# Kernel optimization log

Hardware: AMD Instinct MI355X
Metric: run time of the kernel (lower is better)

Reference implementation:

```python
import jax, jax.numpy as jnp
import numpy as np

B = 1024      # batch of seed nodes
S = 16        # sample_size
H = 256       # hidden
IN = 150      # in_dim + NUM_CLASS (128 + 22)
OUT = 22
HEADS = 8
NN = 100000   # number of graph nodes
LN_EPS = 1e-5


def setup_inputs() -> dict:
    key = jax.random.key(0)
    ks = jax.random.split(key, 16)
    sc = 0.05
    return {
        "node_feats": jax.random.normal(ks[0], (NN, IN), jnp.float32),
        "batch": jax.random.randint(ks[1], (B,), 0, NN),
        "nbr2": jax.random.randint(ks[2], (B, S), 0, NN),
        "nbr1": jax.random.randint(ks[3], (B * (S + 1), S), 0, NN),
        "W_in": jax.random.normal(ks[4], (IN, H), jnp.float32) * sc,
        "b_in": jnp.zeros((H,), jnp.float32),
        "Wqkv": jax.random.normal(ks[5], (2, 3, H, H), jnp.float32) * sc,
        "bqkv": jnp.zeros((2, 3, H), jnp.float32),
        "Wo": jax.random.normal(ks[6], (2, H, H), jnp.float32) * sc,
        "bo": jnp.zeros((2, H), jnp.float32),
        "Wf": jax.random.normal(ks[7], (2, H, H), jnp.float32) * sc,
        "bf": jnp.zeros((2, H), jnp.float32),
        "ln_g": jnp.ones((4, H), jnp.float32),
        "ln_b": jnp.zeros((4, H), jnp.float32),
        "W_out": jax.random.normal(ks[8], (H, OUT), jnp.float32) * sc,
        "b_out": jnp.zeros((OUT,), jnp.float32),
    }


def _layer_norm(x, g, b):
    m = jnp.mean(x, axis=-1, keepdims=True)
    v = jnp.mean((x - m) ** 2, axis=-1, keepdims=True)
    return (x - m) * jax.lax.rsqrt(v + LN_EPS) * g + b


def _mha(q, kv, Wq, Wk, Wv, bq, bk, bv, Wout, bout):
    # q: [N, 1, H], kv: [N, S, H]; single-query multi-head attention
    N, Sk, _ = kv.shape
    dh = H // HEADS
    qp = (q @ Wq + bq).reshape(N, 1, HEADS, dh)
    kp = (kv @ Wk + bk).reshape(N, Sk, HEADS, dh)
    vp = (kv @ Wv + bv).reshape(N, Sk, HEADS, dh)
    att = jax.nn.softmax(
        jnp.einsum("nqhd,nkhd->nhqk", qp, kp) / np.float32(np.sqrt(dh)), axis=-1
    )
    o = jnp.einsum("nhqk,nkhd->nqhd", att, vp).reshape(N, 1, H)
    return o @ Wout + bout


def _attn_block(x, l, Wqkv, bqkv, Wo, bo, Wf, bf, ln_g, ln_b):
    # x: [N, S+1, H]; slot 0 is the query (self), rest are sampled neighbors
    q, kv = x[:, 0:1, :], x[:, 1:, :]
    h = _mha(q, kv, Wqkv[l, 0], Wqkv[l, 1], Wqkv[l, 2],
             bqkv[l, 0], bqkv[l, 1], bqkv[l, 2], Wo[l], bo[l])
    h = h[:, 0, :] + q[:, 0, :]                       # residual
    h = _layer_norm(h, ln_g[2 * l], ln_b[2 * l])
    h = h + (h @ Wf[l] + bf[l])                       # FFN (single Linear) + residual
    return _layer_norm(h, ln_g[2 * l + 1], ln_b[2 * l + 1])


def reference(node_feats, batch, nbr2, nbr1, W_in, b_in, Wqkv, bqkv, Wo, bo,
              Wf, bf, ln_g, ln_b, W_out, b_out):
    # Recursive neighbor expansion (unrolled for layers=2)
    ids1 = jnp.concatenate([batch[:, None], nbr2], axis=1).reshape(-1)   # [B*(S+1)]
    ids0 = jnp.concatenate([ids1[:, None], nbr1], axis=1).reshape(-1)    # [B*(S+1)^2]
    # layer 0: proj_in(features) = ReLU(Linear) (Dropout identity in eval)
    h0 = jax.nn.relu(node_feats[ids0] @ W_in + b_in)                     # [M0, H]
    # layer 1
    h1 = _attn_block(h0.reshape(B * (S + 1), S + 1, H), 0,
                     Wqkv, bqkv, Wo, bo, Wf, bf, ln_g, ln_b)
    # layer 2
    h2 = _attn_block(h1.reshape(B, S + 1, H), 1,
                     Wqkv, bqkv, Wo, bo, Wf, bf, ln_g, ln_b)
    # proj_out: Linear -> Softmax
    return jax.nn.softmax(h2 @ W_out + b_out, axis=-1)
```

## Files before the change

### kernel.cpp

```cpp
#include <hip/hip_runtime.h>
#include <hip/hip_bf16.h>
#include <math.h>

typedef unsigned short ushort_t;
typedef __bf16 bf16x8 __attribute__((ext_vector_type(8)));
typedef float  f32x4  __attribute__((ext_vector_type(4)));

#define B_SZ   1024
#define SEQ    17
#define KVN    16
#define HDIM   256
#define NHEAD  8
#define DH     32
#define INF    150
#define OUTD   22
#define LN_EPS 1e-5f
#define N1     (B_SZ * SEQ)
#define NN_    100000
#define NKVBLK 1563
#define NHQBLK 272

constexpr size_t SZ_H0    = (size_t)NN_ * 256 * 2;
constexpr size_t SZ_KV0   = (size_t)NN_ * 512 * 2;
constexpr size_t SZ_ROW   = (size_t)N1 * 256 * 2;
constexpr size_t OFF_HQ   = 0;
constexpr size_t OFF_KV0  = OFF_HQ + SZ_H0;
constexpr size_t OFF_QKV1 = OFF_KV0;
constexpr size_t OFF_O1   = OFF_QKV1 + (size_t)N1 * 768 * 2;
constexpr size_t OFF_HA2  = OFF_O1 + (size_t)B_SZ * 256 * 2;
constexpr size_t OFF_H2   = OFF_HA2 + (size_t)B_SZ * 256 * 2;
constexpr size_t OFF_Q0   = OFF_KV0 + SZ_KV0;
constexpr size_t OFF_O0   = OFF_Q0 + SZ_ROW;
constexpr size_t OFF_H1   = OFF_O0;
constexpr size_t OFF_HA   = OFF_O0 + SZ_ROW;
constexpr size_t OFF_IDS  = OFF_HA + SZ_ROW;
constexpr size_t OFF_WTIN = OFF_IDS + (size_t)N1 * 4;
constexpr size_t OFF_WKV0 = OFF_WTIN + 256 * 160 * 2;
constexpr size_t OFF_WQ0  = OFF_WKV0 + 512 * 256 * 2;
constexpr size_t OFF_WKVQ1= OFF_WQ0 + 256 * 256 * 2;
constexpr size_t OFF_WO0  = OFF_WKVQ1 + 768 * 256 * 2;
constexpr size_t OFF_WF0  = OFF_WO0 + 256 * 256 * 2;
constexpr size_t OFF_WO1  = OFF_WF0 + 256 * 256 * 2;
constexpr size_t OFF_WF1  = OFF_WO1 + 256 * 256 * 2;
constexpr size_t OFF_B1   = OFF_WF1 + 256 * 256 * 2;

__device__ __forceinline__ ushort_t f2bfu(float x) {
    __hip_bfloat16 h = __float2bfloat16(x);
    return *reinterpret_cast<ushort_t*>(&h);
}
__device__ __forceinline__ float bfu2f(ushort_t u) {
    __hip_bfloat16 h;
    *reinterpret_cast<ushort_t*>(&h) = u;
    return __bfloat162float(h);
}
__device__ __forceinline__ f32x4 mfma16(bf16x8 a, bf16x8 b, f32x4 c) {
    return __builtin_amdgcn_mfma_f32_16x16x32_bf16(a, b, c, 0, 0, 0);
}

__global__ __launch_bounds__(256) void k_prep(
    const float* __restrict__ W_in, const float* __restrict__ Wqkv,
    const float* __restrict__ Wo, const float* __restrict__ Wf,
    const float* __restrict__ bqkv,
    const int* __restrict__ batch, const int* __restrict__ nbr2,
    char* __restrict__ ws) {
    const int job = blockIdx.y;
    const int idx = blockIdx.x * 256 + threadIdx.x;
    if (job == 11) {
        if (idx < N1) {
            int b = idx / SEQ, s = idx % SEQ;
            ((int*)(ws + OFF_IDS))[idx] = (s == 0) ? batch[b] : nbr2[b * KVN + s - 1];
        }
        return;
    }
    if (job == 12) {
        if (idx < 768) ((float*)(ws + OFF_B1))[idx] = bqkv[768 + ((idx + 256) % 768)];
        return;
    }
    const float* src = nullptr; ushort_t* dst = nullptr;
    int Kpad = 256, Kvalid = 256;
    switch (job) {
        case 0:  src = W_in;           dst = (ushort_t*)(ws + OFF_WTIN); Kpad = 160; Kvalid = 150; break;
        case 1:  src = Wqkv + 65536;   dst = (ushort_t*)(ws + OFF_WKV0); break;
        case 2:  src = Wqkv + 131072;  dst = (ushort_t*)(ws + OFF_WKV0) + 65536; break;
        case 3:  src = Wqkv;           dst = (ushort_t*)(ws + OFF_WQ0); break;
        case 4:  src = Wqkv + 262144;  dst = (ushort_t*)(ws + OFF_WKVQ1); break;
        case 5:  src = Wqkv + 327680;  dst = (ushort_t*)(ws + OFF_WKVQ1) + 65536; break;
        case 6:  src = Wqkv + 196608;  dst = (ushort_t*)(ws + OFF_WKVQ1) + 131072; break;
        case 7:  src = Wo;             dst = (ushort_t*)(ws + OFF_WO0); break;
        case 8:  src = Wo + 65536;     dst = (ushort_t*)(ws + OFF_WO1); break;
        case 9:  src = Wf;             dst = (ushort_t*)(ws + OFF_WF0); break;
        case 10: src = Wf + 65536;     dst = (ushort_t*)(ws + OFF_WF1); break;
    }
    const int total = 256 * Kpad;
    if (idx >= total) return;
    int n = idx / Kpad, k = idx % Kpad;
    dst[idx] = (k < Kvalid) ? f2bfu(src[(size_t)k * 256 + n]) : (ushort_t)0;
}

__global__ __launch_bounds__(256) void k_fused(
    const float* __restrict__ nf,
    const ushort_t* __restrict__ Wt_in, const float* __restrict__ b_in,
    const ushort_t* __restrict__ Wkv, const ushort_t* __restrict__ Wq,
    const float* __restrict__ bqkv, const int* __restrict__ ids1,
    ushort_t* __restrict__ kv0, ushort_t* __restrict__ hq,
    ushort_t* __restrict__ q0) {
    __shared__ ushort_t Ah[64 * 256];
    __shared__ ushort_t Sh[4][32][72];
    const int tid = threadIdx.x;
    const bool iskv = blockIdx.x < NKVBLK;
    const int m0 = (iskv ? blockIdx.x : blockIdx.x - NKVBLK) * 64;
    const int lane = tid & 63, w = tid >> 6;
    const int lr = lane & 15, q4 = lane >> 4, lk = q4 * 8;

    {
        ushort_t (*Astage)[168] = reinterpret_cast<ushort_t (*)[168]>(Ah);
        #pragma unroll
        for (int i = 0; i < 5; ++i) {
            int flat = tid + i * 256;
            int row = flat / 20, ch = flat % 20;
            int gm; bool valid;
            if (iskv) { gm = m0 + row; valid = gm < NN_; if (!valid) gm = 0; }
            else      { gm = ids1[m0 + row]; valid = true; }
            const float* ap = nf + (size_t)gm * INF + ch * 8;
            ushort_t tmp[8];
            if (valid && ch < 18) {
                #pragma unroll
                for (int j = 0; j < 4; ++j) {
                    float2 f = *reinterpret_cast<const float2*>(ap + j * 2);
                    tmp[j * 2] = f2bfu(f.x); tmp[j * 2 + 1] = f2bfu(f.y);
                }
            } else {
                #pragma unroll
                for (int j = 0; j < 8; ++j) {
                    int k = ch * 8 + j;
                    tmp[j] = (valid && k < INF) ? f2bfu(ap[j]) : (ushort_t)0;
                }
            }
            *reinterpret_cast<int4*>(&Astage[row][ch * 8]) = *reinterpret_cast<int4*>(tmp);
        }
    }
    __syncthreads();

    f32x4 acc[4][4] = {};
    {
        ushort_t (*Astage)[168] = reinterpret_cast<ushort_t (*)[168]>(Ah);
        #pragma unroll 2
        for (int s = 0; s < 5; ++s) {
            bf16x8 a[4], b[4];
            #pragma unroll
            for (int mi = 0; mi < 4; ++mi)
                a[mi] = *reinterpret_cast<const bf16x8*>(&Astage[mi * 16 + lr][s * 32 + lk]);
            #pragma unroll
            for (int ni = 0; ni < 4; ++ni)
                b[ni] = *reinterpret_cast<const bf16x8*>(
                    Wt_in + (size_t)(w * 64 + ni * 16 + lr) * 160 + s * 32 + lk);
            #pragma unroll
            for (int mi = 0; mi < 4; ++mi)
                #pragma unroll
                for (int ni = 0; ni < 4; ++ni)
                    acc[mi][ni] = mfma16(a[mi], b[ni], acc[mi][ni]);
        }
    }
    __syncthreads();

    #pragma unroll
    for (int ni = 0; ni < 4; ++ni) {
        int col = w * 64 + ni * 16 + lr;
        float bb = b_in[col];
        #pragma unroll
        for (int mi = 0; mi < 4; ++mi)
            #pragma unroll
            for (int r = 0; r < 4; ++r) {
                int row = mi * 16 + q4 * 4 + r;
                Ah[row * 256 + (col ^ ((row & 7) << 3))] =
                    f2bfu(fmaxf(acc[mi][ni][r] + bb, 0.f));
            }
    }
    __syncthreads();

    if (!iskv) {
        #pragma unroll
        for (int i = 0; i < 8; ++i) {
            int flat = tid + i * 256;
            int row = flat >> 5, ch = flat & 31;
            *reinterpret_cast<int4*>(hq + (size_t)(m0 + row) * 256 + ch * 8) =
                *reinterpret_cast<const int4*>(&Ah[row * 256 + (ch ^ (row & 7)) * 8]);
        }
    }

    const int nh = iskv ? 2 : 1;
    for (int h = 0; h < nh; ++h) {
        const ushort_t* Bm = iskv ? (Wkv + (size_t)h * 256 * 256) : Wq;
        const float* bias = iskv ? (bqkv + 256 + h * 256) : bqkv;
        f32x4 acc2[4][4] = {};
        #pragma unroll 2
        for (int s = 0; s < 8; ++s) {
            bf16x8 a[4], b[4];
            #pragma unroll
            for (int mi = 0; mi < 4; ++mi) {
                int row = mi * 16 + lr;
                int chunk = (s * 4 + q4) ^ (row & 7);
                a[mi] = *reinterpret_cast<const bf16x8*>(&Ah[row * 256 + chunk * 8]);
            }
            #pragma unroll
            for (int ni = 0; ni < 4; ++ni)
                b[ni] = *reinterpret_cast<const bf16x8*>(
                    Bm + (size_t)(w * 64 + ni * 16 + lr) * 256 + s * 32 + lk);
            #pragma unroll
            for (int mi = 0; mi < 4; ++mi)
                #pragma unroll
                for (int ni = 0; ni < 4; ++ni)
                    acc2[mi][ni] = mfma16(a[mi], b[ni], acc2[mi][ni]);
        }
        float bl[4];
        #pragma unroll
        for (int ni = 0; ni < 4; ++ni) bl[ni] = bias[w * 64 + ni * 16 + lr];
        ushort_t* outp = iskv ? kv0 : q0;
        const int ldo = iskv ? 512 : 256;
        const int coff = (iskv ? h * 256 : 0) + w * 64;
        #pragma unroll
        for (int part = 0; part < 2; ++part) {
            #pragma unroll
            for (int mi2 = 0; mi2 < 2; ++mi2) {
                int mi = part * 2 + mi2;
                #pragma unroll
                for (int ni = 0; ni < 4; ++ni)
                    #pragma unroll
                    for (int r = 0; r < 4; ++r)
                        Sh[w][mi2 * 16 + q4 * 4 + r][ni * 16 + lr] =
                            f2bfu(acc2[mi][ni][r] + bl[ni]);
            }
            #pragma unroll
            for (int j = 0; j < 4; ++j) {
                int flat = lane + j * 64;
                int r32 = flat >> 3, ch = flat & 7;
                int grow = m0 + part * 32 + r32;
                if (!iskv || grow < NN_)
                    *reinterpret_cast<int4*>(outp + (size_t)grow * ldo + coff + ch * 8) =
                        *reinterpret_cast<const int4*>(&Sh[w][r32][ch * 8]);
            }
        }
    }
}

template<bool RELU>
__global__ __launch_bounds__(256) void gemm64(
    const ushort_t* __restrict__ Asrc, const ushort_t* __restrict__ Bt,
    const float* __restrict__ biasN, ushort_t* __restrict__ out,
    int M, int Ksteps, int lda, int ldb, int ldo,
    const int* __restrict__ arid) {
    __shared__ ushort_t Al[64][40];
    __shared__ ushort_t Bl[64][40];
    const int tid = threadIdx.x;
    const int m0 = blockIdx.x * 64, n0 = blockIdx.y * 64;
    const int lane = tid & 63, w = tid >> 6, wm = w >> 1, wn = w & 1;
    const int srow = tid >> 2, sch = tid & 3;
    const int gmi = m0 + srow;
    const bool valid = gmi < M;
    const int gr = valid ? (arid ? arid[gmi] : gmi) : 0;
    const ushort_t* arow = Asrc + (size_t)gr * lda + sch * 8;
    const ushort_t* brow = Bt + (size_t)(n0 + srow) * ldb + sch * 8;

    int4 aP = {0, 0, 0, 0};
    if (valid) aP = *reinterpret_cast<const int4*>(arow);
    int4 bP = *reinterpret_cast<const int4*>(brow);

    f32x4 acc[2][2] = {};
    for (int s = 0; s < Ksteps; ++s) {
        __syncthreads();
        *reinterpret_cast<int4*>(&Al[srow][sch * 8]) = aP;
        *reinterpret_cast<int4*>(&Bl[srow][sch * 8]) = bP;
        if (s + 1 < Ksteps) {
            if (valid) aP = *reinterpret_cast<const int4*>(arow + (s + 1) * 32);
            bP = *reinterpret_cast<const int4*>(brow + (s + 1) * 32);
        }
        __syncthreads();
        const int lr = lane & 15, lk = (lane >> 4) * 8;
        bf16x8 a0 = *reinterpret_cast<const bf16x8*>(&Al[wm * 32 + lr][lk]);
        bf16x8 a1 = *reinterpret_cast<const bf16x8*>(&Al[wm * 32 + 16 + lr][lk]);
        bf16x8 b0 = *reinterpret_cast<const bf16x8*>(&Bl[wn * 32 + lr][lk]);
        bf16x8 b1 = *reinterpret_cast<const bf16x8*>(&Bl[wn * 32 + 16 + lr][lk]);
        acc[0][0] = mfma16(a0, b0, acc[0][0]);
        acc[0][1] = mfma16(a0, b1, acc[0][1]);
        acc[1][0] = mfma16(a1, b0, acc[1][0]);
        acc[1][1] = mfma16(a1, b1, acc[1][1]);
    }
    #pragma unroll
    for (int mi = 0; mi < 2; ++mi)
        #pragma unroll
        for (int ni = 0; ni < 2; ++ni)
            #pragma unroll
            for (int r = 0; r < 4; ++r) {
                int m = m0 + wm * 32 + mi * 16 + ((lane >> 4) << 2) + r;
                int n = n0 + wn * 32 + ni * 16 + (lane & 15);
                if (m < M) {
                    float v = acc[mi][ni][r] + biasN[n];
                    if (RELU) v = fmaxf(v, 0.f);
                    out[(size_t)m * ldo + n] = f2bfu(v);
                }
            }
}

__global__ __launch_bounds__(256) void gemm_ln(
    const ushort_t* __restrict__ A, const ushort_t* __restrict__ Bt,
    const float* __restrict__ biasN,
    const ushort_t* __restrict__ resmat, const int* __restrict__ residx, int rstride,
    const float* __restrict__ lng, const float* __restrict__ lnb,
    ushort_t* __restrict__ out, int M) {
    __shared__ union {
        struct { ushort_t Al[32][264]; ushort_t Bl[256][40]; } s;
        struct { float xr[32][260]; float mrow[32]; float rrow[32]; int sidx[32]; } e;
    } sm;
    const int tid = threadIdx.x;
    const int m0 = blockIdx.x * 32;
    const int lane = tid & 63, w = tid >> 6;
    const int lr = lane & 15, lk = (lane >> 4) * 8;

    #pragma unroll
    for (int j = 0; j < 4; ++j) {
        int flat = tid + j * 256;
        int row = flat >> 5, ch = flat & 31;
        *reinterpret_cast<int4*>(&sm.s.Al[row][ch * 8]) =
            *reinterpret_cast<const int4*>(A + (size_t)(m0 + row) * 256 + ch * 8);
    }
    const ushort_t* brow = Bt + (size_t)tid * 256;
    int4 bP[4];
    #pragma unroll
    for (int j = 0; j < 4; ++j) bP[j] = *reinterpret_cast<const int4*>(brow + j * 8);

    f32x4 acc[2][4] = {};
    for (int s = 0; s < 8; ++s) {
        __syncthreads();
        #pragma unroll
        for (int j = 0; j < 4; ++j)
            *reinterpret_cast<int4*>(&sm.s.Bl[tid][j * 8]) = bP[j];
        if (s < 7) {
            #pragma unroll
            for (int j = 0; j < 4; ++j)
                bP[j] = *reinterpret_cast<const int4*>(brow + (s + 1) * 32 + j * 8);
        }
        __syncthreads();
        bf16x8 a0 = *reinterpret_cast<const bf16x8*>(&sm.s.Al[lr][s * 32 + lk]);
        bf16x8 a1 = *reinterpret_cast<const bf16x8*>(&sm.s.Al[16 + lr][s * 32 + lk]);
        #pragma unroll
        for (int ni = 0; ni < 4; ++ni) {
            bf16x8 b = *reinterpret_cast<const bf16x8*>(&sm.s.Bl[w * 64 + ni * 16 + lr][lk]);
            acc[0][ni] = mfma16(a0, b, acc[0][ni]);
            acc[1][ni] = mfma16(a1, b, acc[1][ni]);
        }
    }
    __syncthreads();
    if (tid < 32) sm.e.sidx[tid] = residx ? residx[m0 + tid] : (m0 + tid) * rstride;
    #pragma unroll
    for (int mi = 0; mi < 2; ++mi)
        #pragma unroll
        for (int ni = 0; ni < 4; ++ni)
            #pragma unroll
            for (int r = 0; r < 4; ++r) {
                int rl = mi * 16 + ((lane >> 4) << 2) + r;
                int cl = w * 64 + ni * 16 + (lane & 15);
                sm.e.xr[rl][cl] = acc[mi][ni][r];
            }
    __syncthreads();
    {
        float bn = biasN[tid];
        for (int r = 0; r < 32; ++r)
            sm.e.xr[r][tid] += bn + bfu2f(resmat[(size_t)sm.e.sidx[r] * 256 + tid]);
    }
    __syncthreads();
    {
        for (int rr = w * 8; rr < w * 8 + 8; ++rr) {
            float4 v = *reinterpret_cast<const float4*>(&sm.e.xr[rr][lane * 4]);
            float s1 = v.x + v.y + v.z + v.w;
            float s2 = v.x * v.x + v.y * v.y + v.z * v.z + v.w * v.w;
            #pragma unroll
            for (int off = 32; off > 0; off >>= 1) {
                s1 += __shfl_xor(s1, off);
                s2 += __shfl_xor(s2, off);
            }
            if (lane == 0) {
                float m = s1 * (1.f / 256.f);
                float var = s2 * (1.f / 256.f) - m * m;
                sm.e.mrow[rr] = m;
                sm.e.rrow[rr] = rsqrtf(var + LN_EPS);
            }
        }
    }
    __syncthreads();
    {
        float g = lng[tid], b = lnb[tid];
        for (int r = 0; r < 32; ++r) {
            float v = (sm.e.xr[r][tid] - sm.e.mrow[r]) * sm.e.rrow[r] * g + b;
            out[(size_t)(m0 + r) * 256 + tid] = f2bfu(v);
        }
    }
}

__global__ __launch_bounds__(256) void attn_wave(
    const ushort_t* __restrict__ q_all, int qld, int qoff, int qstride,
    const ushort_t* __restrict__ kv_all, int kvld, int koff, int voff,
    const int* __restrict__ kvidx, int ngroups, ushort_t* __restrict__ o_out) {
    __shared__ ushort_t KL[4][KVN][264];
    __shared__ ushort_t VL[4][KVN][264];
    const int w = threadIdx.x >> 6, lane = threadIdx.x & 63;
    const int g = blockIdx.x * 4 + w;
    if (g >= ngroups) return;

    int idx16 = 0;
    if (lane < KVN)
        idx16 = kvidx ? kvidx[g * KVN + lane] : g * SEQ + 1 + lane;

    float qv[4];
    {
        uint2 u = *reinterpret_cast<const uint2*>(
            q_all + (size_t)g * qstride * qld + qoff + lane * 4);
        qv[0] = bfu2f((ushort_t)(u.x & 0xffff));
        qv[1] = bfu2f((ushort_t)(u.x >> 16));
        qv[2] = bfu2f((ushort_t)(u.y & 0xffff));
        qv[3] = bfu2f((ushort_t)(u.y >> 16));
    }
    {
        const int r = lane & 15, qtr = lane >> 4;
        int rid = __shfl(idx16, r);
        const ushort_t* kb = kv_all + (size_t)rid * kvld + koff;
        const ushort_t* vb = kv_all + (size_t)rid * kvld + voff;
        #pragma unroll
        for (int j = 0; j < 8; ++j) {
            int c8 = (qtr * 8 + j) * 8;
            *reinterpret_cast<int4*>(&KL[w][r][c8]) = *reinterpret_cast<const int4*>(kb + c8);
            *reinterpret_cast<int4*>(&VL[w][r][c8]) = *reinterpret_cast<const int4*>(vb + c8);
        }
    }
    float att[KVN];
    #pragma unroll
    for (int k = 0; k < KVN; ++k) {
        uint2 u = *reinterpret_cast<const uint2*>(&KL[w][k][lane * 4]);
        float p = qv[0] * bfu2f((ushort_t)(u.x & 0xffff))
                + qv[1] * bfu2f((ushort_t)(u.x >> 16))
                + qv[2] * bfu2f((ushort_t)(u.y & 0xffff))
                + qv[3] * bfu2f((ushort_t)(u.y >> 16));
        p += __shfl_xor(p, 1);
        p += __shfl_xor(p, 2);
        p += __shfl_xor(p, 4);
        att[k] = p * 0.17677669529663687f;
    }
    float m = att[0];
    #pragma unroll
    for (int k = 1; k < KVN; ++k) m = fmaxf(m, att[k]);
    float sum = 0.f;
    #pragma unroll
    for (int k = 0; k < KVN; ++k) { att[k] = __expf(att[k] - m); sum += att[k]; }
    float inv = 1.f / sum;
    float o[4] = {0.f, 0.f, 0.f, 0.f};
    #pragma unroll
    for (int k = 0; k < KVN; ++k) {
        uint2 u = *reinterpret_cast<const uint2*>(&VL[w][k][lane * 4]);
        float a = att[k] * inv;
        o[0] += a * bfu2f((ushort_t)(u.x & 0xffff));
        o[1] += a * bfu2f((ushort_t)(u.x >> 16));
        o[2] += a * bfu2f((ushort_t)(u.y & 0xffff));
        o[3] += a * bfu2f((ushort_t)(u.y >> 16));
    }
    uint2 r;
    r.x = (unsigned)f2bfu(o[0]) | ((unsigned)f2bfu(o[1]) << 16);
    r.y = (unsigned)f2bfu(o[2]) | ((unsigned)f2bfu(o[3]) << 16);
    *reinterpret_cast<uint2*>(o_out + (size_t)g * 256 + lane * 4) = r;
}

__global__ __launch_bounds__(64) void k_out(
    const ushort_t* __restrict__ h2, const float* __restrict__ W_out,
    const float* __restrict__ b_out, float* __restrict__ out) {
    const int b = blockIdx.x, j = threadIdx.x;
    __shared__ float xr[HDIM];
    for (int k = j; k < HDIM; k += 64) xr[k] = bfu2f(h2[(size_t)b * HDIM + k]);
    __syncthreads();
    float logit = -1e30f;
    if (j < OUTD) {
        float acc = b_out[j];
        for (int k = 0; k < HDIM; ++k) acc += xr[k] * W_out[k * OUTD + j];
        logit = acc;
    }
    float m = logit;
    #pragma unroll
    for (int off = 32; off > 0; off >>= 1) m = fmaxf(m, __shfl_xor(m, off));
    float e = (j < OUTD) ? __expf(logit - m) : 0.f;
    float s = e;
    #pragma unroll
    for (int off = 32; off > 0; off >>= 1) s += __shfl_xor(s, off);
    if (j < OUTD) out[(size_t)b * OUTD + j] = e / s;
}

extern "C" void kernel_launch(void* const* d_in, const int* in_sizes, int n_in,
                              void* d_out, int out_size, void* d_ws, size_t ws_size,
                              hipStream_t stream) {
    const float* nf    = (const float*)d_in[0];
    const int*   batch = (const int*)d_in[1];
    const int*   nbr2  = (const int*)d_in[2];
    const int*   nbr1  = (const int*)d_in[3];
    const float* W_in  = (const float*)d_in[4];
    const float* b_in  = (const float*)d_in[5];
    const float* Wqkv  = (const float*)d_in[6];
    const float* bqkv  = (const float*)d_in[7];
    const float* Wo    = (const float*)d_in[8];
    const float* bo    = (const float*)d_in[9];
    const float* Wf    = (const float*)d_in[10];
    const float* bf    = (const float*)d_in[11];
    const float* ln_g  = (const float*)d_in[12];
    const float* ln_b  = (const float*)d_in[13];
    const float* W_out = (const float*)d_in[14];
    const float* b_out = (const float*)d_in[15];
    float* out = (float*)d_out;
    char* ws = (char*)d_ws;

    ushort_t* hq   = (ushort_t*)(ws + OFF_HQ);
    ushort_t* kv0  = (ushort_t*)(ws + OFF_KV0);
    ushort_t* q0   = (ushort_t*)(ws + OFF_Q0);
    ushort_t* o0   = (ushort_t*)(ws + OFF_O0);
    ushort_t* ha   = (ushort_t*)(ws + OFF_HA);
    ushort_t* h1   = (ushort_t*)(ws + OFF_H1);
    ushort_t* qkv1 = (ushort_t*)(ws + OFF_QKV1);
    ushort_t* o1   = (ushort_t*)(ws + OFF_O1);
    ushort_t* ha2  = (ushort_t*)(ws + OFF_HA2);
    ushort_t* h2   = (ushort_t*)(ws + OFF_H2);
    const int* ids1 = (const int*)(ws + OFF_IDS);

    hipLaunchKernelGGL(k_prep, dim3(256, 13), dim3(256), 0, stream,
                       W_in, Wqkv, Wo, Wf, bqkv, batch, nbr2, ws);
    hipLaunchKernelGGL(k_fused, dim3(NKVBLK + NHQBLK), dim3(256), 0, stream,
                       nf, (const ushort_t*)(ws + OFF_WTIN), b_in,
                       (const ushort_t*)(ws + OFF_WKV0),
                       (const ushort_t*)(ws + OFF_WQ0), bqkv, ids1,
                       kv0, hq, q0);
    hipLaunchKernelGGL(attn_wave, dim3(N1 / 4), dim3(256), 0, stream,
                       q0, 256, 0, 1, kv0, 512, 0, 256, nbr1, N1, o0);
    hipLaunchKernelGGL(gemm_ln, dim3(544), dim3(256), 0, stream,
                       o0, (const ushort_t*)(ws + OFF_WO0), bo,
                       hq, (const int*)nullptr, 1, ln_g, ln_b, ha, N1);
    hipLaunchKernelGGL(gemm_ln, dim3(544), dim3(256), 0, stream,
                       ha, (const ushort_t*)(ws + OFF_WF0), bf,
                       ha, (const int*)nullptr, 1, ln_g + 256, ln_b + 256, h1, N1);
    hipLaunchKernelGGL((gemm64<false>), dim3(272, 12), dim3(256), 0, stream,
                       h1, (const ushort_t*)(ws + OFF_WKVQ1),
                       (const float*)(ws + OFF_B1), qkv1,
                       N1, 8, 256, 256, 768, (const int*)nullptr);
    hipLaunchKernelGGL(attn_wave, dim3(B_SZ / 4), dim3(256), 0, stream,
                       qkv1, 768, 512, 17, qkv1, 768, 0, 256,
                       (const int*)nullptr, B_SZ, o1);
    hipLaunchKernelGGL(gemm_ln, dim3(32), dim3(256), 0, stream,
                       o1, (const ushort_t*)(ws + OFF_WO1), bo + 256,
                       h1, (const int*)nullptr, 17, ln_g + 512, ln_b + 512, ha2, B_SZ);
    hipLaunchKernelGGL(gemm_ln, dim3(32), dim3(256), 0, stream,
                       ha2, (const ushort_t*)(ws + OFF_WF1), bf + 256,
                       ha2, (const int*)nullptr, 1, ln_g + 768, ln_b + 768, h2, B_SZ);
    hipLaunchKernelGGL(k_out, dim3(B_SZ), dim3(64), 0, stream,
                       h2, W_out, b_out, out);
}
```

Before: 337.1 us.

## Fuse Wo+LN and FFN+LN into one kernel, direct-from-global B operands, new QKV1 GEMM

Merges the output-projection+LayerNorm and FFN+LayerNorm kernels into a single k_ffn kernel per attention block. The intermediate row tile stays in shared memory, so the intermediate buffer's global round trip and one launch per layer go away. The B operands (weights) are now read straight from global/L2 into registers with a one-step register prefetch, replacing LDS staging with barriers. The layer-1 QKV projection uses a new 64-row kernel that reuses a swizzled A tile across all three 256-column panels, which cuts repeated A reloads. The trade-offs are more weight traffic through L2 per wave and higher register pressure.

```diff
diff --git a/kernel.cpp b/kernel.cpp
--- a/kernel.cpp
+++ b/kernel.cpp
@@ -27,13 +27,11 @@
 constexpr size_t OFF_KV0  = OFF_HQ + SZ_H0;
 constexpr size_t OFF_QKV1 = OFF_KV0;
 constexpr size_t OFF_O1   = OFF_QKV1 + (size_t)N1 * 768 * 2;
-constexpr size_t OFF_HA2  = OFF_O1 + (size_t)B_SZ * 256 * 2;
-constexpr size_t OFF_H2   = OFF_HA2 + (size_t)B_SZ * 256 * 2;
+constexpr size_t OFF_H2   = OFF_O1 + (size_t)B_SZ * 256 * 2;
 constexpr size_t OFF_Q0   = OFF_KV0 + SZ_KV0;
 constexpr size_t OFF_O0   = OFF_Q0 + SZ_ROW;
 constexpr size_t OFF_H1   = OFF_O0;
-constexpr size_t OFF_HA   = OFF_O0 + SZ_ROW;
-constexpr size_t OFF_IDS  = OFF_HA + SZ_ROW;
+constexpr size_t OFF_IDS  = OFF_O0 + SZ_ROW;
 constexpr size_t OFF_WTIN = OFF_IDS + (size_t)N1 * 4;
 constexpr size_t OFF_WKV0 = OFF_WTIN + 256 * 160 * 2;
 constexpr size_t OFF_WQ0  = OFF_WKV0 + 512 * 256 * 2;
@@ -144,21 +142,33 @@
     f32x4 acc[4][4] = {};
     {
         ushort_t (*Astage)[168] = reinterpret_cast<ushort_t (*)[168]>(Ah);
-        #pragma unroll 2
+        bf16x8 bc[4];
+        #pragma unroll
+        for (int ni = 0; ni < 4; ++ni)
+            bc[ni] = *reinterpret_cast<const bf16x8*>(
+                Wt_in + (size_t)(w * 64 + ni * 16 + lr) * 160 + lk);
+        #pragma unroll
         for (int s = 0; s < 5; ++s) {
-            bf16x8 a[4], b[4];
+            bf16x8 bn[4];
+            if (s < 4) {
+                #pragma unroll
+                for (int ni = 0; ni < 4; ++ni)
+                    bn[ni] = *reinterpret_cast<const bf16x8*>(
+                        Wt_in + (size_t)(w * 64 + ni * 16 + lr) * 160 + (s + 1) * 32 + lk);
+            }
+            bf16x8 a[4];
             #pragma unroll
             for (int mi = 0; mi < 4; ++mi)
                 a[mi] = *reinterpret_cast<const bf16x8*>(&Astage[mi * 16 + lr][s * 32 + lk]);
             #pragma unroll
-            for (int ni = 0; ni < 4; ++ni)
-                b[ni] = *reinterpret_cast<const bf16x8*>(
-                    Wt_in + (size_t)(w * 64 + ni * 16 + lr) * 160 + s * 32 + lk);
-            #pragma unroll
             for (int mi = 0; mi < 4; ++mi)
                 #pragma unroll
                 for (int ni = 0; ni < 4; ++ni)
-                    acc[mi][ni] = mfma16(a[mi], b[ni], acc[mi][ni]);
+                    acc[mi][ni] = mfma16(a[mi], bc[ni], acc[mi][ni]);
+            if (s < 4) {
+                #pragma unroll
+                for (int ni = 0; ni < 4; ++ni) bc[ni] = bn[ni];
+            }
         }
     }
     __syncthreads();
@@ -193,9 +203,21 @@
         const ushort_t* Bm = iskv ? (Wkv + (size_t)h * 256 * 256) : Wq;
         const float* bias = iskv ? (bqkv + 256 + h * 256) : bqkv;
         f32x4 acc2[4][4] = {};
-        #pragma unroll 2
+        bf16x8 bc[4];
+        #pragma unroll
+        for (int ni = 0; ni < 4; ++ni)
+            bc[ni] = *reinterpret_cast<const bf16x8*>(
+                Bm + (size_t)(w * 64 + ni * 16 + lr) * 256 + lk);
+        #pragma unroll
         for (int s = 0; s < 8; ++s) {
-            bf16x8 a[4], b[4];
+            bf16x8 bn[4];
+            if (s < 7) {
+                #pragma unroll
+                for (int ni = 0; ni < 4; ++ni)
+                    bn[ni] = *reinterpret_cast<const bf16x8*>(
+                        Bm + (size_t)(w * 64 + ni * 16 + lr) * 256 + (s + 1) * 32 + lk);
+            }
+            bf16x8 a[4];
             #pragma unroll
             for (int mi = 0; mi < 4; ++mi) {
                 int row = mi * 16 + lr;
@@ -203,14 +225,14 @@
                 a[mi] = *reinterpret_cast<const bf16x8*>(&Ah[row * 256 + chunk * 8]);
             }
             #pragma unroll
-            for (int ni = 0; ni < 4; ++ni)
-                b[ni] = *reinterpret_cast<const bf16x8*>(
-                    Bm + (size_t)(w * 64 + ni * 16 + lr) * 256 + s * 32 + lk);
-            #pragma unroll
             for (int mi = 0; mi < 4; ++mi)
                 #pragma unroll
                 for (int ni = 0; ni < 4; ++ni)
-                    acc2[mi][ni] = mfma16(a[mi], b[ni], acc2[mi][ni]);
+                    acc2[mi][ni] = mfma16(a[mi], bc[ni], acc2[mi][ni]);
+            if (s < 7) {
+                #pragma unroll
+                for (int ni = 0; ni < 4; ++ni) bc[ni] = bn[ni];
+            }
         }
         float bl[4];
         #pragma unroll
@@ -243,134 +265,86 @@
     }
 }
 
-template<bool RELU>
-__global__ __launch_bounds__(256) void gemm64(
-    const ushort_t* __restrict__ Asrc, const ushort_t* __restrict__ Bt,
-    const float* __restrict__ biasN, ushort_t* __restrict__ out,
-    int M, int Ksteps, int lda, int ldb, int ldo,
-    const int* __restrict__ arid) {
-    __shared__ ushort_t Al[64][40];
-    __shared__ ushort_t Bl[64][40];
-    const int tid = threadIdx.x;
-    const int m0 = blockIdx.x * 64, n0 = blockIdx.y * 64;
-    const int lane = tid & 63, w = tid >> 6, wm = w >> 1, wn = w & 1;
-    const int srow = tid >> 2, sch = tid & 3;
-    const int gmi = m0 + srow;
-    const bool valid = gmi < M;
-    const int gr = valid ? (arid ? arid[gmi] : gmi) : 0;
-    const ushort_t* arow = Asrc + (size_t)gr * lda + sch * 8;
-    const ushort_t* brow = Bt + (size_t)(n0 + srow) * ldb + sch * 8;
-
-    int4 aP = {0, 0, 0, 0};
-    if (valid) aP = *reinterpret_cast<const int4*>(arow);
-    int4 bP = *reinterpret_cast<const int4*>(brow);
-
-    f32x4 acc[2][2] = {};
-    for (int s = 0; s < Ksteps; ++s) {
-        __syncthreads();
-        *reinterpret_cast<int4*>(&Al[srow][sch * 8]) = aP;
-        *reinterpret_cast<int4*>(&Bl[srow][sch * 8]) = bP;
-        if (s + 1 < Ksteps) {
-            if (valid) aP = *reinterpret_cast<const int4*>(arow + (s + 1) * 32);
-            bP = *reinterpret_cast<const int4*>(brow + (s + 1) * 32);
-        }
-        __syncthreads();
-        const int lr = lane & 15, lk = (lane >> 4) * 8;
-        bf16x8 a0 = *reinterpret_cast<const bf16x8*>(&Al[wm * 32 + lr][lk]);
-        bf16x8 a1 = *reinterpret_cast<const bf16x8*>(&Al[wm * 32 + 16 + lr][lk]);
-        bf16x8 b0 = *reinterpret_cast<const bf16x8*>(&Bl[wn * 32 + lr][lk]);
-        bf16x8 b1 = *reinterpret_cast<const bf16x8*>(&Bl[wn * 32 + 16 + lr][lk]);
-        acc[0][0] = mfma16(a0, b0, acc[0][0]);
-        acc[0][1] = mfma16(a0, b1, acc[0][1]);
-        acc[1][0] = mfma16(a1, b0, acc[1][0]);
-        acc[1][1] = mfma16(a1, b1, acc[1][1]);
-    }
-    #pragma unroll
-    for (int mi = 0; mi < 2; ++mi)
-        #pragma unroll
-        for (int ni = 0; ni < 2; ++ni)
-            #pragma unroll
-            for (int r = 0; r < 4; ++r) {
-                int m = m0 + wm * 32 + mi * 16 + ((lane >> 4) << 2) + r;
-                int n = n0 + wn * 32 + ni * 16 + (lane & 15);
-                if (m < M) {
-                    float v = acc[mi][ni][r] + biasN[n];
-                    if (RELU) v = fmaxf(v, 0.f);
-                    out[(size_t)m * ldo + n] = f2bfu(v);
-                }
-            }
-}
-
-__global__ __launch_bounds__(256) void gemm_ln(
-    const ushort_t* __restrict__ A, const ushort_t* __restrict__ Bt,
-    const float* __restrict__ biasN,
-    const ushort_t* __restrict__ resmat, const int* __restrict__ residx, int rstride,
-    const float* __restrict__ lng, const float* __restrict__ lnb,
-    ushort_t* __restrict__ out, int M) {
-    __shared__ union {
-        struct { ushort_t Al[32][264]; ushort_t Bl[256][40]; } s;
-        struct { float xr[32][260]; float mrow[32]; float rrow[32]; int sidx[32]; } e;
-    } sm;
+__global__ __launch_bounds__(256) void k_ffn(
+    const ushort_t* __restrict__ Ain, const ushort_t* __restrict__ W1t,
+    const float* __restrict__ b1,
+    const ushort_t* __restrict__ resmat, int rstride,
+    const float* __restrict__ lng1, const float* __restrict__ lnb1,
+    const ushort_t* __restrict__ W2t, const float* __restrict__ b2,
+    const float* __restrict__ lng2, const float* __restrict__ lnb2,
+    ushort_t* __restrict__ out) {
+    __shared__ ushort_t Al[32][264];
+    __shared__ float xr[32][260];
+    __shared__ float mrow[32], rrow[32];
     const int tid = threadIdx.x;
     const int m0 = blockIdx.x * 32;
     const int lane = tid & 63, w = tid >> 6;
-    const int lr = lane & 15, lk = (lane >> 4) * 8;
+    const int lr = lane & 15, q4 = lane >> 4, lk = q4 * 8;
 
     #pragma unroll
     for (int j = 0; j < 4; ++j) {
         int flat = tid + j * 256;
         int row = flat >> 5, ch = flat & 31;
-        *reinterpret_cast<int4*>(&sm.s.Al[row][ch * 8]) =
-            *reinterpret_cast<const int4*>(A + (size_t)(m0 + row) * 256 + ch * 8);
-    }
-    const ushort_t* brow = Bt + (size_t)tid * 256;
-    int4 bP[4];
-    #pragma unroll
-    for (int j = 0; j < 4; ++j) bP[j] = *reinterpret_cast<const int4*>(brow + j * 8);
-
-    f32x4 acc[2][4] = {};
-    for (int s = 0; s < 8; ++s) {
+        *reinterpret_cast<int4*>(&Al[row][ch * 8]) =
+            *reinterpret_cast<const int4*>(Ain + (size_t)(m0 + row) * 256 + ch * 8);
+    }
+    __syncthreads();
+
+    f32x4 acc[2][4];
+    #pragma unroll
+    for (int g = 0; g < 2; ++g) {
+        const ushort_t* Wt = g ? W2t : W1t;
+        #pragma unroll
+        for (int mi = 0; mi < 2; ++mi)
+            #pragma unroll
+            for (int ni = 0; ni < 4; ++ni) acc[mi][ni] = f32x4{0.f, 0.f, 0.f, 0.f};
+        bf16x8 bc[4];
+        #pragma unroll
+        for (int ni = 0; ni < 4; ++ni)
+            bc[ni] = *reinterpret_cast<const bf16x8*>(
+                Wt + (size_t)(w * 64 + ni * 16 + lr) * 256 + lk);
+        #pragma unroll
+        for (int s = 0; s < 8; ++s) {
+            bf16x8 bn[4];
+            if (s < 7) {
+                #pragma unroll
+                for (int ni = 0; ni < 4; ++ni)
+                    bn[ni] = *reinterpret_cast<const bf16x8*>(
+                        Wt + (size_t)(w * 64 + ni * 16 + lr) * 256 + (s + 1) * 32 + lk);
+            }
+            bf16x8 a0 = *reinterpret_cast<const bf16x8*>(&Al[lr][s * 32 + lk]);
+            bf16x8 a1 = *reinterpret_cast<const bf16x8*>(&Al[16 + lr][s * 32 + lk]);
+            #pragma unroll
+            for (int ni = 0; ni < 4; ++ni) {
+                acc[0][ni] = mfma16(a0, bc[ni], acc[0][ni]);
+                acc[1][ni] = mfma16(a1, bc[ni], acc[1][ni]);
+            }
+            if (s < 7) {
+                #pragma unroll
+                for (int ni = 0; ni < 4; ++ni) bc[ni] = bn[ni];
+            }
+        }
+        #pragma unroll
+        for (int mi = 0; mi < 2; ++mi)
+            #pragma unroll
+            for (int ni = 0; ni < 4; ++ni)
+                #pragma unroll
+                for (int r = 0; r < 4; ++r)
+                    xr[mi * 16 + q4 * 4 + r][w * 64 + ni * 16 + lr] = acc[mi][ni][r];
         __syncthreads();
-        #pragma unroll
-        for (int j = 0; j < 4; ++j)
-            *reinterpret_cast<int4*>(&sm.s.Bl[tid][j * 8]) = bP[j];
-        if (s < 7) {
-            #pragma unroll
-            for (int j = 0; j < 4; ++j)
-                bP[j] = *reinterpret_cast<const int4*>(brow + (s + 1) * 32 + j * 8);
+        {
+            float bb = g ? b2[tid] : b1[tid];
+            if (g == 0) {
+                for (int r = 0; r < 32; ++r)
+                    xr[r][tid] += bb + bfu2f(resmat[(size_t)(m0 + r) * rstride * 256 + tid]);
+            } else {
+                for (int r = 0; r < 32; ++r)
+                    xr[r][tid] += bb + bfu2f(Al[r][tid]);
+            }
         }
         __syncthreads();
-        bf16x8 a0 = *reinterpret_cast<const bf16x8*>(&sm.s.Al[lr][s * 32 + lk]);
-        bf16x8 a1 = *reinterpret_cast<const bf16x8*>(&sm.s.Al[16 + lr][s * 32 + lk]);
-        #pragma unroll
-        for (int ni = 0; ni < 4; ++ni) {
-            bf16x8 b = *reinterpret_cast<const bf16x8*>(&sm.s.Bl[w * 64 + ni * 16 + lr][lk]);
-            acc[0][ni] = mfma16(a0, b, acc[0][ni]);
-            acc[1][ni] = mfma16(a1, b, acc[1][ni]);
-        }
-    }
-    __syncthreads();
-    if (tid < 32) sm.e.sidx[tid] = residx ? residx[m0 + tid] : (m0 + tid) * rstride;
-    #pragma unroll
-    for (int mi = 0; mi < 2; ++mi)
-        #pragma unroll
-        for (int ni = 0; ni < 4; ++ni)
-            #pragma unroll
-            for (int r = 0; r < 4; ++r) {
-                int rl = mi * 16 + ((lane >> 4) << 2) + r;
-                int cl = w * 64 + ni * 16 + (lane & 15);
-                sm.e.xr[rl][cl] = acc[mi][ni][r];
-            }
-    __syncthreads();
-    {
-        float bn = biasN[tid];
-        for (int r = 0; r < 32; ++r)
-            sm.e.xr[r][tid] += bn + bfu2f(resmat[(size_t)sm.e.sidx[r] * 256 + tid]);
-    }
-    __syncthreads();
-    {
         for (int rr = w * 8; rr < w * 8 + 8; ++rr) {
-            float4 v = *reinterpret_cast<const float4*>(&sm.e.xr[rr][lane * 4]);
+            float4 v = *reinterpret_cast<const float4*>(&xr[rr][lane * 4]);
             float s1 = v.x + v.y + v.z + v.w;
             float s2 = v.x * v.x + v.y * v.y + v.z * v.z + v.w * v.w;
             #pragma unroll
@@ -381,17 +355,101 @@
             if (lane == 0) {
                 float m = s1 * (1.f / 256.f);
                 float var = s2 * (1.f / 256.f) - m * m;
-                sm.e.mrow[rr] = m;
-                sm.e.rrow[rr] = rsqrtf(var + LN_EPS);
-            }
-        }
+                mrow[rr] = m;
+                rrow[rr] = rsqrtf(var + LN_EPS);
+            }
+        }
+        __syncthreads();
+        if (g == 0) {
+            float gg = lng1[tid], bb = lnb1[tid];
+            for (int r = 0; r < 32; ++r)
+                Al[r][tid] = f2bfu((xr[r][tid] - mrow[r]) * rrow[r] * gg + bb);
+        } else {
+            float gg = lng2[tid], bb = lnb2[tid];
+            for (int r = 0; r < 32; ++r)
+                out[(size_t)(m0 + r) * 256 + tid] =
+                    f2bfu((xr[r][tid] - mrow[r]) * rrow[r] * gg + bb);
+        }
+        __syncthreads();
+    }
+}
+
+__global__ __launch_bounds__(256) void k_qkv1(
+    const ushort_t* __restrict__ h1, const ushort_t* __restrict__ Wt,
+    const float* __restrict__ bias, ushort_t* __restrict__ outm) {
+    __shared__ ushort_t Ah[64 * 256];
+    __shared__ ushort_t Sh[4][32][72];
+    const int tid = threadIdx.x;
+    const int m0 = blockIdx.x * 64;
+    const int lane = tid & 63, w = tid >> 6;
+    const int lr = lane & 15, q4 = lane >> 4, lk = q4 * 8;
+
+    #pragma unroll
+    for (int i = 0; i < 8; ++i) {
+        int flat = tid + i * 256;
+        int row = flat >> 5, ch = flat & 31;
+        *reinterpret_cast<int4*>(&Ah[row * 256 + ((ch ^ (row & 7)) * 8)]) =
+            *reinterpret_cast<const int4*>(h1 + (size_t)(m0 + row) * 256 + ch * 8);
     }
     __syncthreads();
-    {
-        float g = lng[tid], b = lnb[tid];
-        for (int r = 0; r < 32; ++r) {
-            float v = (sm.e.xr[r][tid] - sm.e.mrow[r]) * sm.e.rrow[r] * g + b;
-            out[(size_t)(m0 + r) * 256 + tid] = f2bfu(v);
+
+    for (int p = 0; p < 3; ++p) {
+        f32x4 acc[4][4] = {};
+        bf16x8 bc[4];
+        #pragma unroll
+        for (int ni = 0; ni < 4; ++ni)
+            bc[ni] = *reinterpret_cast<const bf16x8*>(
+                Wt + (size_t)(p * 256 + w * 64 + ni * 16 + lr) * 256 + lk);
+        #pragma unroll
+        for (int s = 0; s < 8; ++s) {
+            bf16x8 bn[4];
+            if (s < 7) {
+                #pragma unroll
+                for (int ni = 0; ni < 4; ++ni)
+                    bn[ni] = *reinterpret_cast<const bf16x8*>(
+                        Wt + (size_t)(p * 256 + w * 64 + ni * 16 + lr) * 256 + (s + 1) * 32 + lk);
+            }
+            bf16x8 a[4];
+            #pragma unroll
+            for (int mi = 0; mi < 4; ++mi) {
+                int row = mi * 16 + lr;
+                int chunk = (s * 4 + q4) ^ (row & 7);
+                a[mi] = *reinterpret_cast<const bf16x8*>(&Ah[row * 256 + chunk * 8]);
+            }
+            #pragma unroll
+            for (int mi = 0; mi < 4; ++mi)
+                #pragma unroll
+                for (int ni = 0; ni < 4; ++ni)
+                    acc[mi][ni] = mfma16(a[mi], bc[ni], acc[mi][ni]);
+            if (s < 7) {
+                #pragma unroll
+                for (int ni = 0; ni < 4; ++ni) bc[ni] = bn[ni];
+            }
+        }
+        float bl[4];
+        #pragma unroll
+        for (int ni = 0; ni < 4; ++ni) bl[ni] = bias[p * 256 + w * 64 + ni * 16 + lr];
+        const int coff = p * 256 + w * 64;
+        #pragma unroll
+        for (int part = 0; part < 2; ++part) {
+            #pragma unroll
+            for (int mi2 = 0; mi2 < 2; ++mi2) {
+                int mi = part * 2 + mi2;
+                #pragma unroll
+                for (int ni = 0; ni < 4; ++ni)
+                    #pragma unroll
+                    for (int r = 0; r < 4; ++r)
+                        Sh[w][mi2 * 16 + q4 * 4 + r][ni * 16 + lr] =
+                            f2bfu(acc[mi][ni][r] + bl[ni]);
+            }
+            #pragma unroll
+            for (int j = 0; j < 4; ++j) {
+                int flat = lane + j * 64;
+                int r32 = flat >> 3, ch = flat & 7;
+                int grow = m0 + part * 32 + r32;
+                *reinterpret_cast<int4*>(outm + (size_t)grow * 768 + coff + ch * 8) =
+                    *reinterpret_cast<const int4*>(&Sh[w][r32][ch * 8]);
+            }
         }
     }
 }
@@ -516,11 +574,9 @@
     ushort_t* kv0  = (ushort_t*)(ws + OFF_KV0);
     ushort_t* q0   = (ushort_t*)(ws + OFF_Q0);
     ushort_t* o0   = (ushort_t*)(ws + OFF_O0);
-    ushort_t* ha   = (ushort_t*)(ws + OFF_HA);
     ushort_t* h1   = (ushort_t*)(ws + OFF_H1);
     ushort_t* qkv1 = (ushort_t*)(ws + OFF_QKV1);
     ushort_t* o1   = (ushort_t*)(ws + OFF_O1);
-    ushort_t* ha2  = (ushort_t*)(ws + OFF_HA2);
     ushort_t* h2   = (ushort_t*)(ws + OFF_H2);
     const int* ids1 = (const int*)(ws + OFF_IDS);
 
@@ -533,25 +589,22 @@
                        kv0, hq, q0);
     hipLaunchKernelGGL(attn_wave, dim3(N1 / 4), dim3(256), 0, stream,
                        q0, 256, 0, 1, kv0, 512, 0, 256, nbr1, N1, o0);
-    hipLaunchKernelGGL(gemm_ln, dim3(544), dim3(256), 0, stream,
+    hipLaunchKernelGGL(k_ffn, dim3(N1 / 32), dim3(256), 0, stream,
                        o0, (const ushort_t*)(ws + OFF_WO0), bo,
-                       hq, (const int*)nullptr, 1, ln_g, ln_b, ha, N1);
-    hipLaunchKernelGGL(gemm_ln, dim3(544), dim3(256), 0, stream,
-                       ha, (const ushort_t*)(ws + OFF_WF0), bf,
-                       ha, (const int*)nullptr, 1, ln_g + 256, ln_b + 256, h1, N1);
-    hipLaunchKernelGGL((gemm64<false>), dim3(272, 12), dim3(256), 0, stream,
+                       hq, 1, ln_g, ln_b,
+                       (const ushort_t*)(ws + OFF_WF0), bf,
+                       ln_g + 256, ln_b + 256, h1);
+    hipLaunchKernelGGL(k_qkv1, dim3(N1 / 64), dim3(256), 0, stream,
                        h1, (const ushort_t*)(ws + OFF_WKVQ1),
-                       (const float*)(ws + OFF_B1), qkv1,
-                       N1, 8, 256, 256, 768, (const int*)nullptr);
+                       (const float*)(ws + OFF_B1), qkv1);
     hipLaunchKernelGGL(attn_wave, dim3(B_SZ / 4), dim3(256), 0, stream,
                        qkv1, 768, 512, 17, qkv1, 768, 0, 256,
                        (const int*)nullptr, B_SZ, o1);
-    hipLaunchKernelGGL(gemm_ln, dim3(32), dim3(256), 0, stream,
+    hipLaunchKernelGGL(k_ffn, dim3(B_SZ / 32), dim3(256), 0, stream,
                        o1, (const ushort_t*)(ws + OFF_WO1), bo + 256,
-                       h1, (const int*)nullptr, 17, ln_g + 512, ln_b + 512, ha2, B_SZ);
-    hipLaunchKernelGGL(gemm_ln, dim3(32), dim3(256), 0, stream,
-                       ha2, (const ushort_t*)(ws + OFF_WF1), bf + 256,
-                       ha2, (const int*)nullptr, 1, ln_g + 768, ln_b + 768, h2, B_SZ);
+                       h1, 17, ln_g + 512, ln_b + 512,
+                       (const ushort_t*)(ws + OFF_WF1), bf + 256,
+                       ln_g + 768, ln_b + 768, h2);
     hipLaunchKernelGGL(k_out, dim3(B_SZ), dim3(64), 0, stream,
                        h2, W_out, b_out, out);
 }
```

Result: faster. 288.4 us (-14.5%).
